# Kernel tuning notes

Hardware: AMD Instinct MI355X
Metric: run time of the kernel (lower is better)

## Reference

```python
import jax, jax.numpy as jnp
import numpy as np

H = 1024          # hidden_size
NH = 16           # num_attention_heads
HD = H // NH      # attention_head_size = 64
B, S = 8, 1024
LN_EPS = 1e-12


def setup_inputs() -> dict:
    key = jax.random.key(0)
    ks = jax.random.split(key, 12)
    sc = 0.02
    return {
        "input_tensor": jax.random.normal(ks[0], (B, S, H), dtype=jnp.float32),
        "attention_mask": jnp.zeros((B, S), dtype=jnp.float32),
        # LinearMem params (quantization disabled -> plain Linear, torch layout [out,in])
        "Wq": jax.random.normal(ks[1], (H, H), dtype=jnp.float32) * sc,
        "bq": jnp.zeros((H,), dtype=jnp.float32),
        "Wk": jax.random.normal(ks[2], (H, H), dtype=jnp.float32) * sc,
        "bk": jnp.zeros((H,), dtype=jnp.float32),
        "Wv": jax.random.normal(ks[3], (H, H), dtype=jnp.float32) * sc,
        "bv": jnp.zeros((H,), dtype=jnp.float32),
        "Wo": jax.random.normal(ks[4], (H, H), dtype=jnp.float32) * sc,
        "bo": jnp.zeros((H,), dtype=jnp.float32),
        "ln_gamma": jnp.ones((H,), dtype=jnp.float32),
        "ln_beta": jnp.zeros((H,), dtype=jnp.float32),
    }


def _heads(x):  # [B,S,H] -> [B,NH,S,HD]
    return x.reshape(B, S, NH, HD).transpose(0, 2, 1, 3)


def reference(input_tensor, attention_mask, Wq, bq, Wk, bk, Wv, bv, Wo, bo, ln_gamma, ln_beta):
    # Q/K/V projections (LinearMem with quantization disabled == Linear)
    q = _heads(jnp.einsum('bsh,oh->bso', input_tensor, Wq) + bq)
    k = _heads(jnp.einsum('bsh,oh->bso', input_tensor, Wk) + bk)
    v = _heads(jnp.einsum('bsh,oh->bso', input_tensor, Wv) + bv)
    scores = jnp.einsum('bnqd,bnkd->bnqk', q, k) / np.float32(np.sqrt(HD))
    scores = scores + attention_mask[:, None, None, :]  # additive mask [B,1,1,S]
    probs = jax.nn.softmax(scores, axis=-1)  # dropout = identity in eval
    ctx = jnp.einsum('bnqk,bnkd->bnqd', probs, v)
    ctx = ctx.transpose(0, 2, 1, 3).reshape(B, S, H)
    # output projection + residual LayerNorm (eps=1e-12)
    out = jnp.einsum('bsh,oh->bso', ctx, Wo) + bo
    resid = out + input_tensor
    mu = jnp.mean(resid, axis=-1, keepdims=True)
    var = jnp.mean(jnp.square(resid - mu), axis=-1, keepdims=True)
    return (resid - mu) * jax.lax.rsqrt(var + LN_EPS) * ln_gamma + ln_beta
```

## Files before the change

### kernel.cpp

```cpp
#include <hip/hip_runtime.h>

#define NHh 16

typedef unsigned short ushortT;
typedef __attribute__((ext_vector_type(8))) short short8;
typedef __attribute__((ext_vector_type(4))) float floatx4;

__device__ __forceinline__ ushortT f2bf(float x) {
    union { float f; unsigned int u; } cv; cv.f = x;
    unsigned int u = cv.u;
    unsigned int r = u + 0x7fffu + ((u >> 16) & 1u);
    return (ushortT)(r >> 16);
}

__device__ __forceinline__ unsigned pack2_trunc(float a, float b) {
    union { float f; unsigned u; } ua, ub;
    ua.f = a; ub.f = b;
    return (ub.u & 0xffff0000u) | (ua.u >> 16);
}

__device__ __forceinline__ void gload_lds16(const ushortT* g, ushortT* l) {
    __builtin_amdgcn_global_load_lds(
        (const __attribute__((address_space(1))) void*)g,
        (__attribute__((address_space(3))) void*)l, 16, 0, 0);
}

__global__ __launch_bounds__(256) void cvt_x(const float* __restrict__ in,
                                             ushortT* __restrict__ out, int n4) {
    int i = blockIdx.x * 256 + threadIdx.x;
    if (i >= n4) return;
    float4 f = ((const float4*)in)[i];
    uint2 o;
    o.x = (unsigned)f2bf(f.x) | ((unsigned)f2bf(f.y) << 16);
    o.y = (unsigned)f2bf(f.z) | ((unsigned)f2bf(f.w) << 16);
    ((uint2*)out)[i] = o;
}

__global__ __launch_bounds__(256) void cvt_w(const float* __restrict__ W0, const float* __restrict__ W1,
                                             const float* __restrict__ W2, const float* __restrict__ W3,
                                             ushortT* __restrict__ o0, ushortT* __restrict__ o1,
                                             ushortT* __restrict__ o2, ushortT* __restrict__ o3, int n4) {
    int z = blockIdx.y;
    const float* in = (z == 0) ? W0 : (z == 1) ? W1 : (z == 2) ? W2 : W3;
    ushortT* out = (z == 0) ? o0 : (z == 1) ? o1 : (z == 2) ? o2 : o3;
    int i = blockIdx.x * 256 + threadIdx.x;
    if (i >= n4) return;
    float4 f = ((const float4*)in)[i];
    uint2 o;
    o.x = (unsigned)f2bf(f.x) | ((unsigned)f2bf(f.y) << 16);
    o.y = (unsigned)f2bf(f.z) | ((unsigned)f2bf(f.w) << 16);
    ((uint2*)out)[i] = o;
}

__device__ __forceinline__ short8 lds_frag(const ushortT* tb, int row, int ks, int qd) {
    int rowblk = row >> 4;
    int r = row & 15;
    int c2 = qd ^ ((r >> 3) << 1);
    return *(const short8*)((const char*)tb + rowblk * 2048 + ks * 1024 + r * 64 + c2 * 16);
}

__device__ __forceinline__ void gemm_loop_256x128(
        const ushortT* __restrict__ Ap, const ushortT* __restrict__ Bp,
        int arow0, int brow0, ushortT* As, ushortT* Bs,
        int tid, int wr, int wc, int qd, int ln, floatx4 (&acc)[4][4]) {
    auto STAGE = [&](int cursor) {
        int kt = cursor >> 2;
        if (kt >= 16) return;
        int h = cursor & 3;
        int buf = kt & 1;
        int k0 = kt << 6;
        if (h < 2) {
            char* L = (char*)As + buf * 32768;
#pragma unroll
            for (int jj = 0; jj < 2; jj++) {
                int o = h * 16384 + jj * 8192 + tid * 16;
                int rowblk = o >> 11, ks = (o >> 10) & 1, r = (o >> 6) & 15;
                int c2 = ((o >> 4) & 3) ^ ((r >> 3) << 1);
                gload_lds16(Ap + (size_t)(arow0 + rowblk * 16 + r) * 1024 + k0 + ks * 32 + c2 * 8,
                            (ushortT*)(L + o));
            }
        } else {
            char* L = (char*)Bs + buf * 16384;
            int o = (h & 1) * 8192 + tid * 16;
            int rowblk = o >> 11, ks = (o >> 10) & 1, r = (o >> 6) & 15;
            int c2 = ((o >> 4) & 3) ^ ((r >> 3) << 1);
            gload_lds16(Bp + (size_t)(brow0 + rowblk * 16 + r) * 1024 + k0 + ks * 32 + c2 * 8,
                        (ushortT*)(L + o));
        }
    };

    for (int c = 0; c < 7; c++) STAGE(c);
    asm volatile("s_waitcnt vmcnt(5)" ::: "memory");
    __builtin_amdgcn_s_barrier();

    short8 afr[2][2], bfr[2][2];
    int cursor = 7;
    for (int T = 0; T < 16; T++) {
        const ushortT* Ab = As + (T & 1) * 16384;
        const ushortT* Bb = Bs + (T & 1) * 8192;
#pragma unroll
        for (int ph = 0; ph < 4; ph++) {
            const int mq = ph >> 1, nq = ph & 1;
#pragma unroll
            for (int ni = 0; ni < 2; ni++)
#pragma unroll
                for (int ks = 0; ks < 2; ks++)
                    bfr[ni][ks] = lds_frag(Bb, nq * 64 + ni * 32 + wc * 16 + ln, ks, qd);
            if (nq == 0) {
#pragma unroll
                for (int mi = 0; mi < 2; mi++)
#pragma unroll
                    for (int ks = 0; ks < 2; ks++)
                        afr[mi][ks] = lds_frag(Ab, (mq * 2 + mi) * 64 + wr * 16 + ln, ks, qd);
            }
            STAGE(cursor); ++cursor;
            __builtin_amdgcn_s_barrier();
            asm volatile("s_waitcnt lgkmcnt(0)" ::: "memory");
            __builtin_amdgcn_s_setprio(1);
#pragma unroll
            for (int mi = 0; mi < 2; mi++)
#pragma unroll
                for (int ni = 0; ni < 2; ni++)
#pragma unroll
                    for (int ks = 0; ks < 2; ks++)
                        acc[mq * 2 + mi][nq * 2 + ni] =
                            __builtin_amdgcn_mfma_f32_16x16x32_bf16(afr[mi][ks], bfr[ni][ks],
                                                                    acc[mq * 2 + mi][nq * 2 + ni], 0, 0, 0);
            __builtin_amdgcn_s_setprio(0);
            if (ph == 3) {
                if (T < 14) { asm volatile("s_waitcnt vmcnt(5)" ::: "memory"); }
                else        { asm volatile("s_waitcnt vmcnt(0)" ::: "memory"); }
            }
            __builtin_amdgcn_s_barrier();
        }
    }
}

__global__ __launch_bounds__(512, 1) void qkv_gemm8(
        const ushortT* __restrict__ X,
        const ushortT* __restrict__ W0, const ushortT* __restrict__ W1, const ushortT* __restrict__ W2,
        const float* __restrict__ b0, const float* __restrict__ b1, const float* __restrict__ b2,
        ushortT* __restrict__ Qo, ushortT* __restrict__ Ko, ushortT* __restrict__ Vo) {
    __shared__ __align__(16) ushortT As[2 * 16384];
    __shared__ __align__(16) ushortT Bs[2 * 8192];

    const int l = blockIdx.x;
    const int xcd = l & 7;
    const int j = l >> 3;
    const int tid = threadIdx.x;
    const int lane = tid & 63;
    const int w = tid >> 6;
    const int wr = w >> 1, wc = w & 1;
    const int qd = lane >> 4, ln = lane & 15;

    int z, arow0, brow0;
    const ushortT* Ap; const ushortT* Bp;
    if (j < 64) {
        z = j >> 5;
        int mg = (j >> 3) & 3;
        int n = j & 7;
        arow0 = (mg * 8 + xcd) * 256;
        brow0 = n * 128;
        Ap = X; Bp = z ? W1 : W0;
    } else {
        z = 2;
        int j2 = j - 64;
        arow0 = (j2 & 3) * 256;
        brow0 = ((j2 >> 2) * 8 + xcd) * 128;
        Ap = W2; Bp = X;
    }

    floatx4 acc[4][4];
#pragma unroll
    for (int i = 0; i < 4; i++)
#pragma unroll
        for (int jj = 0; jj < 4; jj++) acc[i][jj] = (floatx4){0.f, 0.f, 0.f, 0.f};

    gemm_loop_256x128(Ap, Bp, arow0, brow0, As, Bs, tid, wr, wc, qd, ln, acc);

    if (z == 2) {
        floatx4 bv4[4];
#pragma unroll
        for (int mi = 0; mi < 4; mi++)
            bv4[mi] = *(const floatx4*)(b2 + arow0 + mi * 64 + wr * 16 + qd * 4);
#pragma unroll
        for (int ni = 0; ni < 4; ni++) {
            int n = brow0 + ni * 32 + wc * 16 + ln;
            int bb = n >> 10, s = n & 1023;
#pragma unroll
            for (int mi = 0; mi < 4; mi++) {
#pragma unroll
                for (int r2 = 0; r2 < 4; r2++) {
                    int dim = arow0 + mi * 64 + wr * 16 + qd * 4 + r2;
                    int hh = dim >> 6, dd = dim & 63;
                    Vo[((size_t)(bb * NHh + hh) * 64 + dd) * 1024 + s] =
                        f2bf(acc[mi][ni][r2] + bv4[mi][r2]);
                }
            }
        }
    } else {
        ushortT* Out = z ? Ko : Qo;
        const float* bias = z ? b1 : b0;
#pragma unroll
        for (int ni = 0; ni < 4; ni++) {
            int n = brow0 + ni * 32 + wc * 16 + ln;
            float bb = bias[n];
            int h = n >> 6, d = n & 63;
#pragma unroll
            for (int mi = 0; mi < 4; mi++) {
#pragma unroll
                for (int r2 = 0; r2 < 4; r2++) {
                    int m = arow0 + mi * 64 + wr * 16 + qd * 4 + r2;
                    int b = m >> 10, s = m & 1023;
                    Out[(size_t)((b * NHh + h) * 1024 + s) * 64 + d] =
                        f2bf(acc[mi][ni][r2] + bb);
                }
            }
        }
    }
}

__global__ __launch_bounds__(512, 1) void oproj_gemm8(const ushortT* __restrict__ A,
        const ushortT* __restrict__ Wt, const float* __restrict__ bias, float* __restrict__ Pj) {
    __shared__ __align__(16) ushortT As[2 * 16384];
    __shared__ __align__(16) ushortT Bs[2 * 8192];

    const int l = blockIdx.x;
    const int xcd = l & 7;
    const int j = l >> 3;
    const int tid = threadIdx.x;
    const int lane = tid & 63;
    const int w = tid >> 6;
    const int wr = w >> 1, wc = w & 1;
    const int qd = lane >> 4, ln = lane & 15;

    const int arow0 = ((j & 3) * 8 + xcd) * 256;
    const int brow0 = (j >> 2) * 128;

    floatx4 acc[4][4];
#pragma unroll
    for (int i = 0; i < 4; i++)
#pragma unroll
        for (int jj = 0; jj < 4; jj++) acc[i][jj] = (floatx4){0.f, 0.f, 0.f, 0.f};

    gemm_loop_256x128(A, Wt, arow0, brow0, As, Bs, tid, wr, wc, qd, ln, acc);

#pragma unroll
    for (int ni = 0; ni < 4; ni++) {
        int n = brow0 + ni * 32 + wc * 16 + ln;
        float bb = bias[n];
#pragma unroll
        for (int mi = 0; mi < 4; mi++) {
#pragma unroll
            for (int r2 = 0; r2 < 4; r2++) {
                int m = arow0 + mi * 64 + wr * 16 + qd * 4 + r2;
                Pj[(size_t)m * 1024 + n] = acc[mi][ni][r2] + bb;
            }
        }
    }
}

__global__ __launch_bounds__(256, 2) void attn_kernel(const ushortT* __restrict__ Q,
        const ushortT* __restrict__ K, const ushortT* __restrict__ Vg_t,
        const float* __restrict__ mask, ushortT* __restrict__ ctx) {
    __shared__ __align__(16) ushortT Ks[128 * 64];
    __shared__ __align__(16) ushortT Vt[64 * 128];
    __shared__ __align__(16) ushortT Ps[4][64 * 72];

    const int tid = threadIdx.x;
    const int lane = tid & 63;
    const int w = tid >> 6;
    const int qd = lane >> 4;
    const int ln = lane & 15;
    const int l = blockIdx.x;
    const int bh = l & 127;
    const int b = bh >> 4;
    const int h = bh & 15;
    const int qb = l >> 7;

    const ushortT* Qg = Q + (size_t)bh * 65536;
    const ushortT* Kg = K + (size_t)bh * 65536;
    const ushortT* Vg = Vg_t + (size_t)bh * 65536;
    const float* mrow = mask + b * 1024;
    const float LOG2E = 1.4426950408889634f;
    const float SCL = 0.125f * 1.4426950408889634f;

    short8 qf[4][2];
#pragma unroll
    for (int nj = 0; nj < 4; nj++)
#pragma unroll
        for (int ks = 0; ks < 2; ks++)
            qf[nj][ks] = *(const short8*)(Qg + (size_t)(qb * 256 + w * 64 + nj * 16 + ln) * 64 + ks * 32 + qd * 8);

    float lst[4] = {0.f, 0.f, 0.f, 0.f};
    floatx4 accO[4][4];
#pragma unroll
    for (int i = 0; i < 4; i++)
#pragma unroll
        for (int j = 0; j < 4; j++) accO[i][j] = (floatx4){0.f, 0.f, 0.f, 0.f};

    const int ksr = lane >> 3;
    const int kc  = lane & 7;
    const int vdr = lane >> 4;
    const int vcc = lane & 15;

    for (int kt = 0; kt < 8; ++kt) {
        __syncthreads();

#pragma unroll
        for (int ii = 0; ii < 4; ii++) {
            int i = w * 4 + ii;
            int srow = i * 8 + ksr;
            gload_lds16(Kg + (size_t)(kt * 128 + srow) * 64 + (kc ^ ksr) * 8,
                        Ks + i * 512 + lane * 8);
        }
#pragma unroll
        for (int ii = 0; ii < 4; ii++) {
            int i = w * 4 + ii;
            int d = i * 4 + vdr;
            gload_lds16(Vg + (size_t)d * 1024 + kt * 128 + (vcc ^ (d & 15)) * 8,
                        Vt + i * 512 + lane * 8);
        }

        __syncthreads();

#pragma unroll
        for (int h2 = 0; h2 < 2; ++h2) {
            const int s0g = kt * 128 + h2 * 64;

#pragma unroll
            for (int njp = 0; njp < 2; ++njp) {
                floatx4 sv[4][2];
#pragma unroll
                for (int mi = 0; mi < 4; mi++)
#pragma unroll
                    for (int j = 0; j < 2; j++) sv[mi][j] = (floatx4){0.f, 0.f, 0.f, 0.f};
#pragma unroll
                for (int ks = 0; ks < 2; ks++) {
                    short8 af[4];
#pragma unroll
                    for (int mi = 0; mi < 4; mi++)
                        af[mi] = *(const short8*)&Ks[(h2 * 64 + mi * 16 + ln) * 64 +
                                                     (((ks * 4 + qd) ^ (ln & 7)) * 8)];
#pragma unroll
                    for (int mi = 0; mi < 4; mi++)
#pragma unroll
                        for (int j = 0; j < 2; j++)
                            sv[mi][j] = __builtin_amdgcn_mfma_f32_16x16x32_bf16(af[mi], qf[njp * 2 + j][ks], sv[mi][j], 0, 0, 0);
                }

                float rs0 = 0.f, rs1 = 0.f;
#pragma unroll
                for (int mi = 0; mi < 4; mi++) {
                    floatx4 m4 = *(const floatx4*)(mrow + s0g + mi * 16 + qd * 4);
                    float p00 = __builtin_amdgcn_exp2f(sv[mi][0][0] * SCL + m4[0] * LOG2E);
                    float p01 = __builtin_amdgcn_exp2f(sv[mi][0][1] * SCL + m4[1] * LOG2E);
                    float p02 = __builtin_amdgcn_exp2f(sv[mi][0][2] * SCL + m4[2] * LOG2E);
                    float p03 = __builtin_amdgcn_exp2f(sv[mi][0][3] * SCL + m4[3] * LOG2E);
                    float p10 = __builtin_amdgcn_exp2f(sv[mi][1][0] * SCL + m4[0] * LOG2E);
                    float p11 = __builtin_amdgcn_exp2f(sv[mi][1][1] * SCL + m4[1] * LOG2E);
                    float p12 = __builtin_amdgcn_exp2f(sv[mi][1][2] * SCL + m4[2] * LOG2E);
                    float p13 = __builtin_amdgcn_exp2f(sv[mi][1][3] * SCL + m4[3] * LOG2E);
                    rs0 += (p00 + p01) + (p02 + p03);
                    rs1 += (p10 + p11) + (p12 + p13);
                    uint2 w0, w1;
                    w0.x = pack2_trunc(p00, p01); w0.y = pack2_trunc(p02, p03);
                    w1.x = pack2_trunc(p10, p11); w1.y = pack2_trunc(p12, p13);
                    *(uint2*)&Ps[w][(njp * 32 + ln) * 72 + mi * 16 + qd * 4] = w0;
                    *(uint2*)&Ps[w][(njp * 32 + 16 + ln) * 72 + mi * 16 + qd * 4] = w1;
                }
                rs0 += __shfl_xor(rs0, 16, 64); rs0 += __shfl_xor(rs0, 32, 64);
                rs1 += __shfl_xor(rs1, 16, 64); rs1 += __shfl_xor(rs1, 32, 64);
                lst[njp * 2 + 0] += rs0;
                lst[njp * 2 + 1] += rs1;
            }

#pragma unroll
            for (int ks2 = 0; ks2 < 2; ks2++) {
                short8 ap[4], bv[4];
#pragma unroll
                for (int i = 0; i < 4; i++)
                    ap[i] = *(const short8*)&Ps[w][(i * 16 + ln) * 72 + ks2 * 32 + qd * 8];
#pragma unroll
                for (int j = 0; j < 4; j++)
                    bv[j] = *(const short8*)&Vt[(j * 16 + ln) * 128 +
                                                (((h2 * 8 + ks2 * 4 + qd) ^ ln) * 8)];
#pragma unroll
                for (int i = 0; i < 4; i++)
#pragma unroll
                    for (int j = 0; j < 4; j++)
                        accO[i][j] = __builtin_amdgcn_mfma_f32_16x16x32_bf16(ap[i], bv[j], accO[i][j], 0, 0, 0);
            }
        }
    }

#pragma unroll
    for (int i = 0; i < 4; i++) {
#pragma unroll
        for (int r = 0; r < 4; r++) {
            float lv = __shfl(lst[i], qd * 4 + r, 64);
            float linv = 1.f / lv;
            int q = qb * 256 + w * 64 + i * 16 + qd * 4 + r;
#pragma unroll
            for (int j = 0; j < 4; j++) {
                int d = j * 16 + ln;
                ctx[((size_t)(b * 1024 + q)) * 1024 + h * 64 + d] = f2bf(accO[i][j][r] * linv);
            }
        }
    }
}

__global__ __launch_bounds__(256) void ln_kernel(const float* __restrict__ Pj, const float* __restrict__ X,
        const float* __restrict__ gamma, const float* __restrict__ beta, float* __restrict__ out) {
    __shared__ float red[8];
    int row = blockIdx.x;
    int t = threadIdx.x;
    const float4 p4 = ((const float4*)(Pj + (size_t)row * 1024))[t];
    const float4 x4 = ((const float4*)(X + (size_t)row * 1024))[t];
    float r0 = p4.x + x4.x, r1 = p4.y + x4.y, r2 = p4.z + x4.z, r3 = p4.w + x4.w;
    float s = r0 + r1 + r2 + r3;
    float ss = r0 * r0 + r1 * r1 + r2 * r2 + r3 * r3;
#pragma unroll
    for (int o = 1; o < 64; o <<= 1) { s += __shfl_xor(s, o, 64); ss += __shfl_xor(ss, o, 64); }
    int w = t >> 6;
    if ((t & 63) == 0) { red[w] = s; red[4 + w] = ss; }
    __syncthreads();
    s = red[0] + red[1] + red[2] + red[3];
    ss = red[4] + red[5] + red[6] + red[7];
    float mu = s * (1.f / 1024.f);
    float var = ss * (1.f / 1024.f) - mu * mu;
    float inv = rsqrtf(var + 1e-12f);
    const float4 g4 = ((const float4*)gamma)[t];
    const float4 b4 = ((const float4*)beta)[t];
    float4 o4;
    o4.x = (r0 - mu) * inv * g4.x + b4.x;
    o4.y = (r1 - mu) * inv * g4.y + b4.y;
    o4.z = (r2 - mu) * inv * g4.z + b4.z;
    o4.w = (r3 - mu) * inv * g4.w + b4.w;
    ((float4*)(out + (size_t)row * 1024))[t] = o4;
}

extern "C" void kernel_launch(void* const* d_in, const int* in_sizes, int n_in,
                              void* d_out, int out_size, void* d_ws, size_t ws_size,
                              hipStream_t stream) {
    const float* x     = (const float*)d_in[0];
    const float* mask  = (const float*)d_in[1];
    const float* Wq    = (const float*)d_in[2];
    const float* bq    = (const float*)d_in[3];
    const float* Wk    = (const float*)d_in[4];
    const float* bk    = (const float*)d_in[5];
    const float* Wv    = (const float*)d_in[6];
    const float* bv    = (const float*)d_in[7];
    const float* Wo    = (const float*)d_in[8];
    const float* bo    = (const float*)d_in[9];
    const float* gamma = (const float*)d_in[10];
    const float* beta  = (const float*)d_in[11];
    float* out = (float*)d_out;

    char* ws = (char*)d_ws;
    ushortT* Xb  = (ushortT*)(ws);
    ushortT* Wqb = (ushortT*)(ws + (16u << 20));
    ushortT* Wkb = (ushortT*)(ws + (18u << 20));
    ushortT* Wvb = (ushortT*)(ws + (20u << 20));
    ushortT* Wob = (ushortT*)(ws + (22u << 20));
    ushortT* Qb  = (ushortT*)(ws + (24u << 20));
    ushortT* Kb  = (ushortT*)(ws + (40u << 20));
    ushortT* Vb  = (ushortT*)(ws + (56u << 20));
    ushortT* Cb  = (ushortT*)(ws);
    float*   Pj  = (float*)(ws + (24u << 20));

    cvt_x<<<8192, 256, 0, stream>>>(x, Xb, 2097152);
    cvt_w<<<dim3(1024, 4), 256, 0, stream>>>(Wq, Wk, Wv, Wo, Wqb, Wkb, Wvb, Wob, 262144);
    qkv_gemm8<<<768, 512, 0, stream>>>(Xb, Wqb, Wkb, Wvb, bq, bk, bv, Qb, Kb, Vb);
    attn_kernel<<<512, 256, 0, stream>>>(Qb, Kb, Vb, mask, Cb);
    oproj_gemm8<<<256, 512, 0, stream>>>(Cb, Wob, bo, Pj);
    ln_kernel<<<8192, 256, 0, stream>>>(Pj, x, gamma, beta, out);
}
```

Before: 299.4 us.

## Triple-buffer GEMM LDS tiles with one barrier pair per K-tile

Replaces the double-buffered GEMM main loop, which had four phases per K-tile, with a triple-buffered loop. Each K-tile issues its whole next-next tile prefetch at once, loads all A/B fragments, then runs 32 MFMAs between a single pair of barriers. Global source pointers and LDS offsets are precomputed once instead of recomputed per stage. This cuts the barrier count and the address arithmetic, and gives loads a longer prefetch distance. In exchange it uses 144KB of LDS and more VGPRs for the 16 fragment registers.

```diff
diff --git a/kernel.cpp b/kernel.cpp
--- a/kernel.cpp
+++ b/kernel.cpp
@@ -52,97 +52,101 @@
     ((uint2*)out)[i] = o;
 }
 
-__device__ __forceinline__ short8 lds_frag(const ushortT* tb, int row, int ks, int qd) {
-    int rowblk = row >> 4;
-    int r = row & 15;
-    int c2 = qd ^ ((r >> 3) << 1);
-    return *(const short8*)((const char*)tb + rowblk * 2048 + ks * 1024 + r * 64 + c2 * 16);
-}
-
-__device__ __forceinline__ void gemm_loop_256x128(
+__device__ __forceinline__ void gemm_core_256x128(
         const ushortT* __restrict__ Ap, const ushortT* __restrict__ Bp,
-        int arow0, int brow0, ushortT* As, ushortT* Bs,
+        int arow0, int brow0, ushortT* As3, ushortT* Bs3,
         int tid, int wr, int wc, int qd, int ln, floatx4 (&acc)[4][4]) {
-    auto STAGE = [&](int cursor) {
-        int kt = cursor >> 2;
-        if (kt >= 16) return;
-        int h = cursor & 3;
-        int buf = kt & 1;
-        int k0 = kt << 6;
-        if (h < 2) {
-            char* L = (char*)As + buf * 32768;
-#pragma unroll
-            for (int jj = 0; jj < 2; jj++) {
-                int o = h * 16384 + jj * 8192 + tid * 16;
-                int rowblk = o >> 11, ks = (o >> 10) & 1, r = (o >> 6) & 15;
-                int c2 = ((o >> 4) & 3) ^ ((r >> 3) << 1);
-                gload_lds16(Ap + (size_t)(arow0 + rowblk * 16 + r) * 1024 + k0 + ks * 32 + c2 * 8,
-                            (ushortT*)(L + o));
-            }
-        } else {
-            char* L = (char*)Bs + buf * 16384;
-            int o = (h & 1) * 8192 + tid * 16;
-            int rowblk = o >> 11, ks = (o >> 10) & 1, r = (o >> 6) & 15;
-            int c2 = ((o >> 4) & 3) ^ ((r >> 3) << 1);
-            gload_lds16(Bp + (size_t)(brow0 + rowblk * 16 + r) * 1024 + k0 + ks * 32 + c2 * 8,
-                        (ushortT*)(L + o));
-        }
-    };
-
-    for (int c = 0; c < 7; c++) STAGE(c);
-    asm volatile("s_waitcnt vmcnt(5)" ::: "memory");
+    const ushortT* srcA[4]; const ushortT* srcB[2];
+    int oA[4], oB[2];
+#pragma unroll
+    for (int k = 0; k < 4; k++) {
+        int o = k * 8192 + tid * 16;
+        int rowblk = o >> 11, ks = (o >> 10) & 1, r = (o >> 6) & 15;
+        int c2 = ((o >> 4) & 3) ^ ((r >> 3) << 1);
+        srcA[k] = Ap + (size_t)(arow0 + rowblk * 16 + r) * 1024 + ks * 32 + c2 * 8;
+        oA[k] = o;
+    }
+#pragma unroll
+    for (int k = 0; k < 2; k++) {
+        int o = k * 8192 + tid * 16;
+        int rowblk = o >> 11, ks = (o >> 10) & 1, r = (o >> 6) & 15;
+        int c2 = ((o >> 4) & 3) ^ ((r >> 3) << 1);
+        srcB[k] = Bp + (size_t)(brow0 + rowblk * 16 + r) * 1024 + ks * 32 + c2 * 8;
+        oB[k] = o;
+    }
+#pragma unroll
+    for (int t = 0; t < 2; t++) {
+#pragma unroll
+        for (int k = 0; k < 4; k++) {
+            gload_lds16(srcA[k], (ushortT*)((char*)As3 + t * 32768 + oA[k]));
+            srcA[k] += 64;
+        }
+#pragma unroll
+        for (int k = 0; k < 2; k++) {
+            gload_lds16(srcB[k], (ushortT*)((char*)Bs3 + t * 16384 + oB[k]));
+            srcB[k] += 64;
+        }
+    }
+    asm volatile("s_waitcnt vmcnt(6)" ::: "memory");
     __builtin_amdgcn_s_barrier();
 
-    short8 afr[2][2], bfr[2][2];
-    int cursor = 7;
+    const int lnc = ln * 64 + ((qd ^ ((ln >> 3) << 1)) * 16);
+
+    int bi = 0, si = 2;
     for (int T = 0; T < 16; T++) {
-        const ushortT* Ab = As + (T & 1) * 16384;
-        const ushortT* Bb = Bs + (T & 1) * 8192;
-#pragma unroll
-        for (int ph = 0; ph < 4; ph++) {
-            const int mq = ph >> 1, nq = ph & 1;
-#pragma unroll
-            for (int ni = 0; ni < 2; ni++)
+        const char* Ab = (const char*)As3 + bi * 32768;
+        const char* Bb = (const char*)Bs3 + bi * 16384;
+        short8 afr[4][2], bfr[4][2];
+#pragma unroll
+        for (int mi = 0; mi < 4; mi++)
+#pragma unroll
+            for (int ks = 0; ks < 2; ks++)
+                afr[mi][ks] = *(const short8*)(Ab + (mi * 4 + wr) * 2048 + ks * 1024 + lnc);
+#pragma unroll
+        for (int ni = 0; ni < 4; ni++)
+#pragma unroll
+            for (int ks = 0; ks < 2; ks++)
+                bfr[ni][ks] = *(const short8*)(Bb + (ni * 2 + wc) * 2048 + ks * 1024 + lnc);
+        if (T < 14) {
+#pragma unroll
+            for (int k = 0; k < 4; k++) {
+                gload_lds16(srcA[k], (ushortT*)((char*)As3 + si * 32768 + oA[k]));
+                srcA[k] += 64;
+            }
+#pragma unroll
+            for (int k = 0; k < 2; k++) {
+                gload_lds16(srcB[k], (ushortT*)((char*)Bs3 + si * 16384 + oB[k]));
+                srcB[k] += 64;
+            }
+        }
+        __builtin_amdgcn_s_barrier();
+        asm volatile("s_waitcnt lgkmcnt(0)" ::: "memory");
+        __builtin_amdgcn_sched_barrier(0);
+        __builtin_amdgcn_s_setprio(1);
+#pragma unroll
+        for (int mi = 0; mi < 4; mi++)
+#pragma unroll
+            for (int ni = 0; ni < 4; ni++)
 #pragma unroll
                 for (int ks = 0; ks < 2; ks++)
-                    bfr[ni][ks] = lds_frag(Bb, nq * 64 + ni * 32 + wc * 16 + ln, ks, qd);
-            if (nq == 0) {
-#pragma unroll
-                for (int mi = 0; mi < 2; mi++)
-#pragma unroll
-                    for (int ks = 0; ks < 2; ks++)
-                        afr[mi][ks] = lds_frag(Ab, (mq * 2 + mi) * 64 + wr * 16 + ln, ks, qd);
-            }
-            STAGE(cursor); ++cursor;
-            __builtin_amdgcn_s_barrier();
-            asm volatile("s_waitcnt lgkmcnt(0)" ::: "memory");
-            __builtin_amdgcn_s_setprio(1);
-#pragma unroll
-            for (int mi = 0; mi < 2; mi++)
-#pragma unroll
-                for (int ni = 0; ni < 2; ni++)
-#pragma unroll
-                    for (int ks = 0; ks < 2; ks++)
-                        acc[mq * 2 + mi][nq * 2 + ni] =
-                            __builtin_amdgcn_mfma_f32_16x16x32_bf16(afr[mi][ks], bfr[ni][ks],
-                                                                    acc[mq * 2 + mi][nq * 2 + ni], 0, 0, 0);
-            __builtin_amdgcn_s_setprio(0);
-            if (ph == 3) {
-                if (T < 14) { asm volatile("s_waitcnt vmcnt(5)" ::: "memory"); }
-                else        { asm volatile("s_waitcnt vmcnt(0)" ::: "memory"); }
-            }
-            __builtin_amdgcn_s_barrier();
-        }
-    }
-}
-
-__global__ __launch_bounds__(512, 1) void qkv_gemm8(
+                    acc[mi][ni] = __builtin_amdgcn_mfma_f32_16x16x32_bf16(
+                        afr[mi][ks], bfr[ni][ks], acc[mi][ni], 0, 0, 0);
+        __builtin_amdgcn_s_setprio(0);
+        if (T < 14) { asm volatile("s_waitcnt vmcnt(6)" ::: "memory"); }
+        else        { asm volatile("s_waitcnt vmcnt(0)" ::: "memory"); }
+        __builtin_amdgcn_s_barrier();
+        bi = (bi == 2) ? 0 : bi + 1;
+        si = (si == 2) ? 0 : si + 1;
+    }
+}
+
+__global__ __launch_bounds__(512, 1) void qkv_gemm3(
         const ushortT* __restrict__ X,
         const ushortT* __restrict__ W0, const ushortT* __restrict__ W1, const ushortT* __restrict__ W2,
         const float* __restrict__ b0, const float* __restrict__ b1, const float* __restrict__ b2,
         ushortT* __restrict__ Qo, ushortT* __restrict__ Ko, ushortT* __restrict__ Vo) {
-    __shared__ __align__(16) ushortT As[2 * 16384];
-    __shared__ __align__(16) ushortT Bs[2 * 8192];
+    __shared__ __align__(16) ushortT As3[3 * 16384];
+    __shared__ __align__(16) ushortT Bs3[3 * 8192];
 
     const int l = blockIdx.x;
     const int xcd = l & 7;
@@ -176,7 +180,7 @@
 #pragma unroll
         for (int jj = 0; jj < 4; jj++) acc[i][jj] = (floatx4){0.f, 0.f, 0.f, 0.f};
 
-    gemm_loop_256x128(Ap, Bp, arow0, brow0, As, Bs, tid, wr, wc, qd, ln, acc);
+    gemm_core_256x128(Ap, Bp, arow0, brow0, As3, Bs3, tid, wr, wc, qd, ln, acc);
 
     if (z == 2) {
         floatx4 bv4[4];
@@ -220,10 +224,10 @@
     }
 }
 
-__global__ __launch_bounds__(512, 1) void oproj_gemm8(const ushortT* __restrict__ A,
+__global__ __launch_bounds__(512, 1) void oproj_gemm3(const ushortT* __restrict__ A,
         const ushortT* __restrict__ Wt, const float* __restrict__ bias, float* __restrict__ Pj) {
-    __shared__ __align__(16) ushortT As[2 * 16384];
-    __shared__ __align__(16) ushortT Bs[2 * 8192];
+    __shared__ __align__(16) ushortT As3[3 * 16384];
+    __shared__ __align__(16) ushortT Bs3[3 * 8192];
 
     const int l = blockIdx.x;
     const int xcd = l & 7;
@@ -243,7 +247,7 @@
 #pragma unroll
         for (int jj = 0; jj < 4; jj++) acc[i][jj] = (floatx4){0.f, 0.f, 0.f, 0.f};
 
-    gemm_loop_256x128(A, Wt, arow0, brow0, As, Bs, tid, wr, wc, qd, ln, acc);
+    gemm_core_256x128(A, Wt, arow0, brow0, As3, Bs3, tid, wr, wc, qd, ln, acc);
 
 #pragma unroll
     for (int ni = 0; ni < 4; ni++) {
@@ -471,8 +475,8 @@
 
     cvt_x<<<8192, 256, 0, stream>>>(x, Xb, 2097152);
     cvt_w<<<dim3(1024, 4), 256, 0, stream>>>(Wq, Wk, Wv, Wo, Wqb, Wkb, Wvb, Wob, 262144);
-    qkv_gemm8<<<768, 512, 0, stream>>>(Xb, Wqb, Wkb, Wvb, bq, bk, bv, Qb, Kb, Vb);
+    qkv_gemm3<<<768, 512, 0, stream>>>(Xb, Wqb, Wkb, Wvb, bq, bk, bv, Qb, Kb, Vb);
     attn_kernel<<<512, 256, 0, stream>>>(Qb, Kb, Vb, mask, Cb);
-    oproj_gemm8<<<256, 512, 0, stream>>>(Cb, Wob, bo, Pj);
+    oproj_gemm3<<<256, 512, 0, stream>>>(Cb, Wob, bo, Pj);
     ln_kernel<<<8192, 256, 0, stream>>>(Pj, x, gamma, beta, out);
 }
```

New measurement: 289.0 us. -3.5%, faster.
